# Kernel tuning notes

Measured on AMD Instinct MI355X. Metric: run time of the kernel, lower is better.

Reference implementation:

```python
import jax, jax.numpy as jnp
import numpy as np

B, N, R = 8, 1024, 8192
D_IN, REL_D = 32, 1
NF_P, NF_R, NF_E, D_OUT = 128, 128, 128, 3
PSTEP = 3


def setup_inputs() -> dict:
    key = jax.random.key(0)
    ks = jax.random.split(key, 26)
    state = jax.random.normal(ks[0], (B, N, D_IN), dtype=jnp.float32)
    # Rr/Rs are one-hot selection matrices [B, N, R]: column j selects the
    # receiver/sender particle of relation j.
    recv = jax.random.randint(ks[1], (B, R), 0, N)
    send = jax.random.randint(ks[2], (B, R), 0, N)
    Rr = jnp.transpose(jax.nn.one_hot(recv, N, dtype=jnp.float32), (0, 2, 1))
    Rs = jnp.transpose(jax.nn.one_hot(send, N, dtype=jnp.float32), (0, 2, 1))
    Ra = jax.random.normal(ks[3], (B, R, REL_D), dtype=jnp.float32)

    def lin(k, i, o):
        kw, kb = jax.random.split(k)
        return (0.02 * jax.random.normal(kw, (i, o), dtype=jnp.float32),
                0.02 * jax.random.normal(kb, (o,), dtype=jnp.float32))

    pe_w0, pe_b0 = lin(ks[4], D_IN, NF_P)
    pe_w1, pe_b1 = lin(ks[5], NF_P, NF_E)
    re_w0, re_b0 = lin(ks[6], 2 * D_IN + REL_D, NF_R)
    re_w1, re_b1 = lin(ks[7], NF_R, NF_R)
    re_w2, re_b2 = lin(ks[8], NF_R, NF_R)
    rp_w, rp_b = lin(ks[9], NF_R + 2 * NF_E, NF_E)   # relation_propagator
    pp_w, pp_b = lin(ks[10], 2 * NF_E, NF_E)          # particle_propagator
    pr_w0, pr_b0 = lin(ks[11], NF_E, NF_E)            # particle_predictor
    pr_w1, pr_b1 = lin(ks[12], NF_E, D_OUT)
    return dict(state=state, Rr=Rr, Rs=Rs, Ra=Ra, pstep=PSTEP,
                pe_w0=pe_w0, pe_b0=pe_b0, pe_w1=pe_w1, pe_b1=pe_b1,
                re_w0=re_w0, re_b0=re_b0, re_w1=re_w1, re_b1=re_b1,
                re_w2=re_w2, re_b2=re_b2, rp_w=rp_w, rp_b=rp_b,
                pp_w=pp_w, pp_b=pp_b, pr_w0=pr_w0, pr_b0=pr_b0,
                pr_w1=pr_w1, pr_b1=pr_b1)


def reference(state, Rr, Rs, Ra, pstep,
              pe_w0, pe_b0, pe_w1, pe_b1,
              re_w0, re_b0, re_w1, re_b1, re_w2, re_b2,
              rp_w, rp_b, pp_w, pp_b,
              pr_w0, pr_b0, pr_w1, pr_b1):
    relu = jax.nn.relu
    # gather particle states into relation slots: Rr^T @ state -> [B, R, D]
    state_r = jnp.einsum('bnr,bnd->brd', Rr, state)
    state_s = jnp.einsum('bnr,bnd->brd', Rs, state)
    # particle encoder: Linear-ReLU-Linear-ReLU
    particle_encode = relu(relu(state @ pe_w0 + pe_b0) @ pe_w1 + pe_b1)  # [B,N,NF_E]
    # relation encoder: 3-layer MLP with ReLU after each layer
    rel_in = jnp.concatenate([state_r, state_s, Ra], axis=2)
    h = relu(rel_in @ re_w0 + re_b0)
    h = relu(h @ re_w1 + re_b1)
    relation_encode = relu(h @ re_w2 + re_b2)  # [B,R,NF_R]

    particle_effect = jnp.zeros((B, N, NF_E), dtype=state.dtype)
    for _ in range(pstep):
        effect_r = jnp.einsum('bnr,bne->bre', Rr, particle_effect)  # gather
        effect_s = jnp.einsum('bnr,bne->bre', Rs, particle_effect)
        rel_x = jnp.concatenate([relation_encode, effect_r, effect_s], axis=2)
        relation_effect = relu(rel_x @ rp_w + rp_b)  # [B,R,NF_E]
        # scatter-add relation effects back to receiver particles
        effect_agg = jnp.einsum('bnr,bre->bne', Rr, relation_effect)
        part_x = jnp.concatenate([particle_encode, effect_agg], axis=2)
        # residual particle propagator: relu(linear(x) + prev_effect)
        particle_effect = relu(part_x @ pp_w + pp_b + particle_effect)
    pred = relu(particle_effect @ pr_w0 + pr_b0) @ pr_w1 + pr_b1  # [B,N,D_OUT]
    return pred
```

## Files before the change

kernel.cpp:

```cpp
#include <hip/hip_runtime.h>

#define NB 8
#define NP 1024
#define NR 8192

typedef unsigned short u16;
typedef __attribute__((ext_vector_type(8))) short bf16x8;
typedef __attribute__((ext_vector_type(4))) float f32x4;
typedef __attribute__((ext_vector_type(4))) unsigned int u32x4;

#define MFMA __builtin_amdgcn_mfma_f32_16x16x32_bf16

static __device__ __forceinline__ float bf2f(u16 u) {
    union { unsigned int i; float f; } v; v.i = ((unsigned int)u) << 16; return v.f;
}
static __device__ __forceinline__ unsigned int f2bf(float f) {
    union { float fv; unsigned int i; } v; v.fv = f;
    unsigned int r = v.i + 0x7FFFu + ((v.i >> 16) & 1u);
    return r >> 16;
}
static __device__ __forceinline__ unsigned int pack2(float a, float b) {
    return f2bf(a) | (f2bf(b) << 16);
}
static __device__ __forceinline__ void unpk8(uint4 v, float* o) {
    o[0] = bf2f((u16)(v.x & 0xFFFF)); o[1] = bf2f((u16)(v.x >> 16));
    o[2] = bf2f((u16)(v.y & 0xFFFF)); o[3] = bf2f((u16)(v.y >> 16));
    o[4] = bf2f((u16)(v.z & 0xFFFF)); o[5] = bf2f((u16)(v.z >> 16));
    o[6] = bf2f((u16)(v.w & 0xFFFF)); o[7] = bf2f((u16)(v.w >> 16));
}

__global__ __launch_bounds__(256) void k_idxprep(
    const u32x4* __restrict__ Rr4, const u32x4* __restrict__ Rs4,
    u16* __restrict__ recv, u16* __restrict__ send,
    const float* __restrict__ w0, const float* __restrict__ w1,
    const float* __restrict__ w2, const float* __restrict__ w3,
    const float* __restrict__ w4, const float* __restrict__ w5,
    const float* __restrict__ w6, const float* __restrict__ w7,
    bf16x8* __restrict__ wfrag)
{
    int tid = threadIdx.x;
    if (blockIdx.x < 8) {
        const float* W; int KC, kv, off;
        switch (blockIdx.x) {
            case 0:  W = w0; KC = 3;  kv = 65;  off = 0;  break;
            case 1:  W = w1; KC = 4;  kv = 128; off = 6;  break;
            case 2:  W = w2; KC = 4;  kv = 128; off = 14; break;
            case 3:  W = w3; KC = 1;  kv = 32;  off = 22; break;
            case 4:  W = w4; KC = 4;  kv = 128; off = 24; break;
            case 5:  W = w5; KC = 12; kv = 384; off = 32; break;
            case 6:  W = w6; KC = 8;  kv = 256; off = 56; break;
            default: W = w7; KC = 4;  kv = 128; off = 72; break;
        }
        int wave = tid >> 6, quad = (tid >> 4) & 3, l16 = tid & 15;
        for (int kc = 0; kc < KC; ++kc)
          for (int nt = 0; nt < 2; ++nt) {
            bf16x8 f;
            #pragma unroll
            for (int j = 0; j < 8; ++j) {
                int k = kc*32 + quad*8 + j;
                f[j] = (k < kv) ? (short)f2bf(W[k*128 + wave*32 + nt*16 + l16]) : (short)0;
            }
            wfrag[(off + kc*2 + nt)*256 + tid] = f;
          }
        return;
    }
    int sid = blockIdx.x - 8;
    int mat = sid & 1;
    const u32x4* src = mat ? Rs4 : Rr4;
    u16* dst = mat ? send : recv;
    long base = (long)(sid >> 1) * 512;
    long i0 = base + tid;
    long i1 = base + 256 + tid;
    u32x4 v0 = __builtin_nontemporal_load(src + i0);
    u32x4 v1 = __builtin_nontemporal_load(src + i1);
    {
        int c4 = (int)(i0 & 2047), n = (int)((i0 >> 11) & 1023), b = (int)(i0 >> 21);
        int o = b * NR + c4 * 4;
        if (v0[0]) dst[o + 0] = (u16)n;
        if (v0[1]) dst[o + 1] = (u16)n;
        if (v0[2]) dst[o + 2] = (u16)n;
        if (v0[3]) dst[o + 3] = (u16)n;
    }
    {
        int c4 = (int)(i1 & 2047), n = (int)((i1 >> 11) & 1023), b = (int)(i1 >> 21);
        int o = b * NR + c4 * 4;
        if (v1[0]) dst[o + 0] = (u16)n;
        if (v1[1]) dst[o + 1] = (u16)n;
        if (v1[2]) dst[o + 2] = (u16)n;
        if (v1[3]) dst[o + 3] = (u16)n;
    }
}

__global__ __launch_bounds__(1024) void k_csr(
    const u16* __restrict__ recv, const u16* __restrict__ send,
    int* __restrict__ row_ptr, u16* __restrict__ pos,
    u16* __restrict__ send_sorted)
{
    __shared__ int s[NP];
    __shared__ int cur[NP];
    int b = blockIdx.x, t = threadIdx.x;
    cur[t] = 0;
    __syncthreads();
    int pv[NR / 1024];
    #pragma unroll
    for (int k = 0; k < NR / 1024; ++k) {
        pv[k] = recv[b * NR + k * 1024 + t] & 1023;
        atomicAdd(&cur[pv[k]], 1);
    }
    __syncthreads();
    int v = cur[t];
    s[t] = v;
    __syncthreads();
    #pragma unroll
    for (int off = 1; off < NP; off <<= 1) {
        int add = (t >= off) ? s[t - off] : 0;
        __syncthreads();
        s[t] += add;
        __syncthreads();
    }
    int excl = s[t] - v;
    row_ptr[b * (NP + 1) + t] = excl;
    cur[t] = excl;
    if (t == NP - 1) row_ptr[b * (NP + 1) + NP] = s[t];
    __syncthreads();
    #pragma unroll
    for (int k = 0; k < NR / 1024; ++k) {
        int r = k * 1024 + t;
        int j = atomicAdd(&cur[pv[k]], 1) & 8191;
        pos[b * NR + r] = (u16)j;
        send_sorted[b * NR + j] = send[b * NR + r];
    }
}

template<int KC>
static __device__ __forceinline__ void load_wfrag(
    const bf16x8* __restrict__ fb, bf16x8 (&wf)[KC][2], int tid)
{
    #pragma unroll
    for (int kc = 0; kc < KC; ++kc)
      #pragma unroll
      for (int nt = 0; nt < 2; ++nt)
        wf[kc][nt] = fb[(kc*2 + nt)*256 + tid];
}

template<int MT, int KC, int LDA>
static __device__ __forceinline__ void mfma_compute(
    const u16* xlds, const bf16x8 (&wf)[KC][2], f32x4 (&acc)[MT][2],
    int l16, int quad)
{
    #pragma unroll
    for (int kc = 0; kc < KC; ++kc) {
        bf16x8 a[MT];
        #pragma unroll
        for (int mt = 0; mt < MT; ++mt)
            a[mt] = *(const bf16x8*)(xlds + (mt*16 + l16)*LDA + kc*32 + quad*8);
        #pragma unroll
        for (int mt = 0; mt < MT; ++mt) {
            acc[mt][0] = MFMA(a[mt], wf[kc][0], acc[mt][0], 0, 0, 0);
            acc[mt][1] = MFMA(a[mt], wf[kc][1], acc[mt][1], 0, 0, 0);
        }
    }
}

template<int MT>
static __device__ __forceinline__ void zero_acc(f32x4 (&acc)[MT][2]) {
    #pragma unroll
    for (int mt = 0; mt < MT; ++mt)
      #pragma unroll
      for (int nt = 0; nt < 2; ++nt)
        acc[mt][nt] = f32x4{0.f, 0.f, 0.f, 0.f};
}

template<int MT, int LDA>
static __device__ __forceinline__ void store_c_lds(
    u16* xlds, const f32x4 (&acc)[MT][2], const float* __restrict__ bias,
    int wave, int quad, int l16, int coloff = 0)
{
    #pragma unroll
    for (int mt = 0; mt < MT; ++mt)
      #pragma unroll
      for (int nt = 0; nt < 2; ++nt) {
        int col = wave*32 + nt*16 + l16;
        float bv = bias[col];
        #pragma unroll
        for (int rg = 0; rg < 4; ++rg)
            xlds[(mt*16 + quad*4 + rg)*LDA + coloff + col] =
                (u16)f2bf(fmaxf(acc[mt][nt][rg] + bv, 0.f));
      }
}

template<int MT, bool RELU>
static __device__ __forceinline__ void store_c_glob(
    u16* __restrict__ out, long row0, const f32x4 (&acc)[MT][2],
    const float* __restrict__ bias, int wave, int quad, int l16)
{
    #pragma unroll
    for (int mt = 0; mt < MT; ++mt)
      #pragma unroll
      for (int nt = 0; nt < 2; ++nt) {
        int col = wave*32 + nt*16 + l16;
        float bv = bias[col];
        #pragma unroll
        for (int rg = 0; rg < 4; ++rg) {
            long r = row0 + mt*16 + quad*4 + rg;
            float v = acc[mt][nt][rg] + bv;
            if (RELU) v = fmaxf(v, 0.f);
            out[r*128 + col] = (u16)f2bf(v);
        }
      }
}

__global__ __launch_bounds__(256) void k_encpe(
    const float* __restrict__ state, const float* __restrict__ Ra,
    const u16* __restrict__ recv, const u16* __restrict__ send,
    const u16* __restrict__ pos,
    const bf16x8* __restrict__ f_re0, const float* __restrict__ re_b0,
    const bf16x8* __restrict__ f_re1, const float* __restrict__ re_b1,
    const bf16x8* __restrict__ f_re2, const float* __restrict__ re_b2,
    const bf16x8* __restrict__ f_rpP, const float* __restrict__ rp_b,
    u16* __restrict__ bufP,
    const bf16x8* __restrict__ f_pe0, const float* __restrict__ pe_b0,
    const bf16x8* __restrict__ f_pe1, const float* __restrict__ pe_b1,
    u16* __restrict__ penc)
{
    constexpr int LDA = 136;
    __shared__ __align__(16) u16 xlds[64 * LDA];
    const int tid = threadIdx.x;
    const int wave = tid >> 6, quad = (tid >> 4) & 3, l16 = tid & 15;
    f32x4 acc[4][2];

    if (blockIdx.x < 1024) {
        const int row0 = blockIdx.x * 64;
        const int b = row0 >> 13;
        {
            int r = tid >> 2, tt = tid & 3;
            int rel = row0 + r;
            u16* dst = xlds + r * LDA;
            int ri = recv[rel] & 1023;
            int si = send[rel] & 1023;
            const float* rrow = state + ((long)(b*NP + ri)) * 32;
            const float* srow = state + ((long)(b*NP + si)) * 32;
            float4 a0 = *(const float4*)(rrow + tt*8);
            float4 a1 = *(const float4*)(rrow + tt*8 + 4);
            uint4 o;
            o.x = pack2(a0.x, a0.y); o.y = pack2(a0.z, a0.w);
            o.z = pack2(a1.x, a1.y); o.w = pack2(a1.z, a1.w);
            *(uint4*)(dst + tt*8) = o;
            float4 s0 = *(const float4*)(srow + tt*8);
            float4 s1 = *(const float4*)(srow + tt*8 + 4);
            o.x = pack2(s0.x, s0.y); o.y = pack2(s0.z, s0.w);
            o.z = pack2(s1.x, s1.y); o.w = pack2(s1.z, s1.w);
            *(uint4*)(dst + 32 + tt*8) = o;
            if (tt == 3) {
                uint4 z = make_uint4(0, 0, 0, 0);
                *(uint4*)(dst + 64) = z; *(uint4*)(dst + 72) = z;
                *(uint4*)(dst + 80) = z; *(uint4*)(dst + 88) = z;
                dst[64] = (u16)f2bf(Ra[rel]);
            }
        }
        __syncthreads();
        zero_acc<4>(acc);
        {
            bf16x8 wf[3][2];
            load_wfrag<3>(f_re0, wf, tid);
            mfma_compute<4, 3, LDA>(xlds, wf, acc, l16, quad);
        }
        __syncthreads();
        store_c_lds<4, LDA>(xlds, acc, re_b0, wave, quad, l16);
        __syncthreads();
        zero_acc<4>(acc);
        {
            bf16x8 wf[4][2];
            load_wfrag<4>(f_re1, wf, tid);
            mfma_compute<4, 4, LDA>(xlds, wf, acc, l16, quad);
        }
        __syncthreads();
        store_c_lds<4, LDA>(xlds, acc, re_b1, wave, quad, l16);
        __syncthreads();
        zero_acc<4>(acc);
        {
            bf16x8 wf[4][2];
            load_wfrag<4>(f_re2, wf, tid);
            mfma_compute<4, 4, LDA>(xlds, wf, acc, l16, quad);
        }
        __syncthreads();
        store_c_lds<4, LDA>(xlds, acc, re_b2, wave, quad, l16);
        __syncthreads();
        zero_acc<4>(acc);
        {
            bf16x8 wf[4][2];
            load_wfrag<4>(f_rpP, wf, tid);
            mfma_compute<4, 4, LDA>(xlds, wf, acc, l16, quad);
        }
        #pragma unroll
        for (int mt = 0; mt < 4; ++mt)
          #pragma unroll
          for (int nt = 0; nt < 2; ++nt) {
            int col = wave*32 + nt*16 + l16;
            float bv = rp_b[col];
            #pragma unroll
            for (int rg = 0; rg < 4; ++rg) {
                int rl = mt*16 + quad*4 + rg;
                int j = pos[row0 + rl] & 8191;
                bufP[((long)(b*NR + j))*128 + col] = (u16)f2bf(acc[mt][nt][rg] + bv);
            }
          }
    } else {
        const long row0 = (long)(blockIdx.x - 1024) * 64;
        for (int idx = tid; idx < 64 * 8; idx += 256) {
            int r = idx >> 3, c = idx & 7;
            float4 v = *(const float4*)(state + (row0 + r)*32 + c*4);
            uint2 o; o.x = pack2(v.x, v.y); o.y = pack2(v.z, v.w);
            *(uint2*)(xlds + r*LDA + c*4) = o;
        }
        __syncthreads();
        zero_acc<4>(acc);
        {
            bf16x8 wf[1][2];
            load_wfrag<1>(f_pe0, wf, tid);
            mfma_compute<4, 1, LDA>(xlds, wf, acc, l16, quad);
        }
        __syncthreads();
        store_c_lds<4, LDA>(xlds, acc, pe_b0, wave, quad, l16);
        __syncthreads();
        zero_acc<4>(acc);
        {
            bf16x8 wf[4][2];
            load_wfrag<4>(f_pe1, wf, tid);
            mfma_compute<4, 4, LDA>(xlds, wf, acc, l16, quad);
        }
        store_c_glob<4, true>(penc, row0, acc, pe_b1, wave, quad, l16);
    }
}

template<bool STEP1, bool MAKEUV, bool LAST>
__global__ __launch_bounds__(256) void k_pp(
    const u16* __restrict__ penc, const u16* __restrict__ bufP,
    const u16* __restrict__ UV_in, u16* __restrict__ UV_out,
    const int* __restrict__ row_ptr, const u16* __restrict__ send_sorted,
    const bf16x8* __restrict__ f_pp, const float* __restrict__ pp_b,
    const bf16x8* __restrict__ f_U, const bf16x8* __restrict__ f_V,
    const bf16x8* __restrict__ f_pr0, const float* __restrict__ pr_b0,
    const float* __restrict__ pr_w1, const float* __restrict__ pr_b1,
    float* __restrict__ peff32_io, float* __restrict__ out)
{
    constexpr int LDA = 264;
    __shared__ __align__(16) u16 xlds[32 * LDA];
    const int tid = threadIdx.x;
    const int wave = tid >> 6, quad = (tid >> 4) & 3, l16 = tid & 15;
    const long row0 = (long)blockIdx.x * 32;

    for (int idx = tid; idx < 512; idx += 256) {
        int r = idx >> 4, c = idx & 15;
        *(uint4*)(xlds + r*LDA + c*8) = *(const uint4*)(penc + (row0 + r)*128 + c*8);
    }
    {
        int pp = tid >> 3;
        int cq = tid & 7;
        int gp = (int)row0 + pp;
        int b = gp >> 10, pl = gp & 1023;
        const int* rp = row_ptr + b * (NP + 1);
        int s0 = rp[pl], e0 = rp[pl + 1];
        float a[16];
        #pragma unroll
        for (int t = 0; t < 16; ++t) a[t] = 0.f;
        float uv[16];
        if (!STEP1) {
            const u16* ur = UV_in + ((long)gp)*256 + cq*16;
            unpk8(*(const uint4*)ur, uv);
            unpk8(*(const uint4*)(ur + 8), uv + 8);
        }
        for (int j = s0; j < e0; ++j) {
            const u16* prow = bufP + ((long)(b*NR + j))*128 + cq*16;
            float pv[16];
            unpk8(*(const uint4*)prow, pv);
            unpk8(*(const uint4*)(prow + 8), pv + 8);
            if (STEP1) {
                #pragma unroll
                for (int e = 0; e < 16; ++e) a[e] += fmaxf(pv[e], 0.f);
            } else {
                int sj = send_sorted[b * NR + j] & 1023;
                const u16* vrow = UV_in + ((long)(b*NP + sj))*256 + 128 + cq*16;
                float vv[16];
                unpk8(*(const uint4*)vrow, vv);
                unpk8(*(const uint4*)(vrow + 8), vv + 8);
                #pragma unroll
                for (int e = 0; e < 16; ++e)
                    a[e] += fmaxf(pv[e] + uv[e] + vv[e], 0.f);
            }
        }
        u16* dst = xlds + pp*LDA + 128 + cq*16;
        uint4 o;
        o.x = pack2(a[0], a[1]);   o.y = pack2(a[2], a[3]);
        o.z = pack2(a[4], a[5]);   o.w = pack2(a[6], a[7]);
        *(uint4*)dst = o;
        o.x = pack2(a[8], a[9]);   o.y = pack2(a[10], a[11]);
        o.z = pack2(a[12], a[13]); o.w = pack2(a[14], a[15]);
        *(uint4*)(dst + 8) = o;
    }
    __syncthreads();

    f32x4 acc[2][2];
    {
        bf16x8 wf[8][2];
        load_wfrag<8>(f_pp, wf, tid);
        zero_acc<2>(acc);
        mfma_compute<2, 8, LDA>(xlds, wf, acc, l16, quad);
    }
    __syncthreads();

    #pragma unroll
    for (int mt = 0; mt < 2; ++mt)
      #pragma unroll
      for (int nt = 0; nt < 2; ++nt) {
        int col = wave*32 + nt*16 + l16;
        float bv = pp_b[col];
        #pragma unroll
        for (int rg = 0; rg < 4; ++rg) {
            int rloc = mt*16 + quad*4 + rg;
            long r = row0 + rloc;
            float prev = STEP1 ? 0.f : peff32_io[r*128 + col];
            float v = fmaxf(acc[mt][nt][rg] + bv + prev, 0.f);
            if (!LAST) peff32_io[r*128 + col] = v;
            xlds[rloc*LDA + col] = (u16)f2bf(v);
        }
      }
    __syncthreads();

    if (MAKEUV) {
        #pragma unroll
        for (int half = 0; half < 2; ++half) {
            bf16x8 wf[4][2];
            load_wfrag<4>(half ? f_V : f_U, wf, tid);
            zero_acc<2>(acc);
            mfma_compute<2, 4, LDA>(xlds, wf, acc, l16, quad);
            #pragma unroll
            for (int mt = 0; mt < 2; ++mt)
              #pragma unroll
              for (int nt = 0; nt < 2; ++nt) {
                int col = half*128 + wave*32 + nt*16 + l16;
                #pragma unroll
                for (int rg = 0; rg < 4; ++rg) {
                    long r = row0 + mt*16 + quad*4 + rg;
                    UV_out[r*256 + col] = (u16)f2bf(acc[mt][nt][rg]);
                }
              }
        }
    }
    if (LAST) {
        bf16x8 wf[4][2];
        load_wfrag<4>(f_pr0, wf, tid);
        zero_acc<2>(acc);
        mfma_compute<2, 4, LDA>(xlds, wf, acc, l16, quad);
        store_c_lds<2, LDA>(xlds, acc, pr_b0, wave, quad, l16, 128);
        __syncthreads();
        if (tid < 96) {
            int row = tid / 3, col = tid - row * 3;
            float s = pr_b1[col];
            const u16* hr = xlds + row * LDA + 128;
            #pragma unroll 8
            for (int k = 0; k < 128; ++k) s += bf2f(hr[k]) * pr_w1[k*3 + col];
            out[(row0 + row)*3 + col] = s;
        }
    }
}

extern "C" void kernel_launch(void* const* d_in, const int* in_sizes, int n_in,
                              void* d_out, int out_size, void* d_ws, size_t ws_size,
                              hipStream_t stream) {
    const float* state = (const float*)d_in[0];
    const float* Rr    = (const float*)d_in[1];
    const float* Rs    = (const float*)d_in[2];
    const float* Ra    = (const float*)d_in[3];
    const float* pe_w0 = (const float*)d_in[5];
    const float* pe_b0 = (const float*)d_in[6];
    const float* pe_w1 = (const float*)d_in[7];
    const float* pe_b1 = (const float*)d_in[8];
    const float* re_w0 = (const float*)d_in[9];
    const float* re_b0 = (const float*)d_in[10];
    const float* re_w1 = (const float*)d_in[11];
    const float* re_b1 = (const float*)d_in[12];
    const float* re_w2 = (const float*)d_in[13];
    const float* re_b2 = (const float*)d_in[14];
    const float* rp_w  = (const float*)d_in[15];
    const float* rp_b  = (const float*)d_in[16];
    const float* pp_w  = (const float*)d_in[17];
    const float* pp_b  = (const float*)d_in[18];
    const float* pr_w0 = (const float*)d_in[19];
    const float* pr_b0 = (const float*)d_in[20];
    const float* pr_w1 = (const float*)d_in[21];
    const float* pr_b1 = (const float*)d_in[22];

    char* p = (char*)d_ws;
    u16*    bufP    = (u16*)p;    p += (size_t)NB*NR*128*2;
    u16*    UVa     = (u16*)p;    p += (size_t)NB*NP*256*2;
    u16*    UVb     = (u16*)p;    p += (size_t)NB*NP*256*2;
    float*  peff32  = (float*)p;  p += (size_t)NB*NP*128*4;
    u16*    penc    = (u16*)p;    p += (size_t)NB*NP*128*2;
    bf16x8* wfrag   = (bf16x8*)p; p += (size_t)80*256*16;
    int*    row_ptr = (int*)p;    p += (size_t)NB*(NP+1)*4 + 12;
    u16*    recv    = (u16*)p;    p += (size_t)NB*NR*2;
    u16*    send    = (u16*)p;    p += (size_t)NB*NR*2;
    u16*    pos     = (u16*)p;    p += (size_t)NB*NR*2;
    u16*    send_s  = (u16*)p;    p += (size_t)NB*NR*2;

    const bf16x8* f_re0 = wfrag + 0*256;
    const bf16x8* f_re1 = wfrag + 6*256;
    const bf16x8* f_re2 = wfrag + 14*256;
    const bf16x8* f_pe0 = wfrag + 22*256;
    const bf16x8* f_pe1 = wfrag + 24*256;
    const bf16x8* f_rpP = wfrag + 32*256;
    const bf16x8* f_rpU = wfrag + 40*256;
    const bf16x8* f_rpV = wfrag + 48*256;
    const bf16x8* f_pp  = wfrag + 56*256;
    const bf16x8* f_pr0 = wfrag + 72*256;

    float* outp = (float*)d_out;

    k_idxprep<<<65544, 256, 0, stream>>>((const u32x4*)Rr, (const u32x4*)Rs, recv, send,
                                         re_w0, re_w1, re_w2, pe_w0, pe_w1, rp_w, pp_w, pr_w0,
                                         wfrag);
    k_csr<<<NB, 1024, 0, stream>>>(recv, send, row_ptr, pos, send_s);
    k_encpe<<<1152, 256, 0, stream>>>(state, Ra, recv, send, pos,
                                      f_re0, re_b0, f_re1, re_b1, f_re2, re_b2,
                                      f_rpP, rp_b, bufP,
                                      f_pe0, pe_b0, f_pe1, pe_b1, penc);
    k_pp<true,  true,  false><<<256, 256, 0, stream>>>(
        penc, bufP, UVa, UVa, row_ptr, send_s, f_pp, pp_b,
        f_rpU, f_rpV, f_pr0, pr_b0, pr_w1, pr_b1, peff32, outp);
    k_pp<false, true,  false><<<256, 256, 0, stream>>>(
        penc, bufP, UVa, UVb, row_ptr, send_s, f_pp, pp_b,
        f_rpU, f_rpV, f_pr0, pr_b0, pr_w1, pr_b1, peff32, outp);
    k_pp<false, false, true><<<256, 256, 0, stream>>>(
        penc, bufP, UVb, UVa, row_ptr, send_s, f_pp, pp_b,
        f_rpU, f_rpV, f_pr0, pr_b0, pr_w1, pr_b1, peff32, outp);
}
```

Baseline: 621.8 us.

## Move particle encoder into index-prep kernel and widen one-hot scan per block

Particle-encoder blocks move from the relation-encoder kernel into the index-prep kernel, converting fp32 weights to bf16 inline so they no longer depend on the packed weight fragments. The one-hot scan now has each block load 8 vectors per thread, which cuts the grid from about 65k to about 16k blocks. The CSR prefix scan switches from a shared-memory Hillis-Steele loop to wave shuffle scans. The propagation gather prefetches send indices eight at a time and broadcasts them with shuffles. The cost is more shared memory in the index-prep kernel, which may lower its occupancy.

```diff
diff --git a/kernel.cpp b/kernel.cpp
--- a/kernel.cpp
+++ b/kernel.cpp
@@ -27,6 +27,84 @@
     o[2] = bf2f((u16)(v.y & 0xFFFF)); o[3] = bf2f((u16)(v.y >> 16));
     o[4] = bf2f((u16)(v.z & 0xFFFF)); o[5] = bf2f((u16)(v.z >> 16));
     o[6] = bf2f((u16)(v.w & 0xFFFF)); o[7] = bf2f((u16)(v.w >> 16));
+}
+
+template<int KC>
+static __device__ __forceinline__ void load_wfrag(
+    const bf16x8* __restrict__ fb, bf16x8 (&wf)[KC][2], int tid)
+{
+    #pragma unroll
+    for (int kc = 0; kc < KC; ++kc)
+      #pragma unroll
+      for (int nt = 0; nt < 2; ++nt)
+        wf[kc][nt] = fb[(kc*2 + nt)*256 + tid];
+}
+
+template<int MT, int KC, int LDA>
+static __device__ __forceinline__ void mfma_compute(
+    const u16* xlds, const bf16x8 (&wf)[KC][2], f32x4 (&acc)[MT][2],
+    int l16, int quad)
+{
+    #pragma unroll
+    for (int kc = 0; kc < KC; ++kc) {
+        bf16x8 a[MT];
+        #pragma unroll
+        for (int mt = 0; mt < MT; ++mt)
+            a[mt] = *(const bf16x8*)(xlds + (mt*16 + l16)*LDA + kc*32 + quad*8);
+        #pragma unroll
+        for (int mt = 0; mt < MT; ++mt) {
+            acc[mt][0] = MFMA(a[mt], wf[kc][0], acc[mt][0], 0, 0, 0);
+            acc[mt][1] = MFMA(a[mt], wf[kc][1], acc[mt][1], 0, 0, 0);
+        }
+    }
+}
+
+template<int MT>
+static __device__ __forceinline__ void zero_acc(f32x4 (&acc)[MT][2]) {
+    #pragma unroll
+    for (int mt = 0; mt < MT; ++mt)
+      #pragma unroll
+      for (int nt = 0; nt < 2; ++nt)
+        acc[mt][nt] = f32x4{0.f, 0.f, 0.f, 0.f};
+}
+
+template<int MT, int LDA>
+static __device__ __forceinline__ void store_c_lds(
+    u16* xlds, const f32x4 (&acc)[MT][2], const float* __restrict__ bias,
+    int wave, int quad, int l16, int coloff = 0)
+{
+    #pragma unroll
+    for (int mt = 0; mt < MT; ++mt)
+      #pragma unroll
+      for (int nt = 0; nt < 2; ++nt) {
+        int col = wave*32 + nt*16 + l16;
+        float bv = bias[col];
+        #pragma unroll
+        for (int rg = 0; rg < 4; ++rg)
+            xlds[(mt*16 + quad*4 + rg)*LDA + coloff + col] =
+                (u16)f2bf(fmaxf(acc[mt][nt][rg] + bv, 0.f));
+      }
+}
+
+template<int MT, bool RELU>
+static __device__ __forceinline__ void store_c_glob(
+    u16* __restrict__ out, long row0, const f32x4 (&acc)[MT][2],
+    const float* __restrict__ bias, int wave, int quad, int l16)
+{
+    #pragma unroll
+    for (int mt = 0; mt < MT; ++mt)
+      #pragma unroll
+      for (int nt = 0; nt < 2; ++nt) {
+        int col = wave*32 + nt*16 + l16;
+        float bv = bias[col];
+        #pragma unroll
+        for (int rg = 0; rg < 4; ++rg) {
+            long r = row0 + mt*16 + quad*4 + rg;
+            float v = acc[mt][nt][rg] + bv;
+            if (RELU) v = fmaxf(v, 0.f);
+            out[r*128 + col] = (u16)f2bf(v);
+        }
+      }
 }
 
 __global__ __launch_bounds__(256) void k_idxprep(
@@ -36,9 +114,15 @@
     const float* __restrict__ w2, const float* __restrict__ w3,
     const float* __restrict__ w4, const float* __restrict__ w5,
     const float* __restrict__ w6, const float* __restrict__ w7,
-    bf16x8* __restrict__ wfrag)
-{
+    bf16x8* __restrict__ wfrag,
+    const float* __restrict__ state, const float* __restrict__ pe_b0,
+    const float* __restrict__ pe_b1, u16* __restrict__ penc)
+{
+    constexpr int LDA = 136;
+    __shared__ __align__(16) u16 xlds[64 * LDA];
     int tid = threadIdx.x;
+    const int wave = tid >> 6, quad = (tid >> 4) & 3, l16 = tid & 15;
+
     if (blockIdx.x < 8) {
         const float* W; int KC, kv, off;
         switch (blockIdx.x) {
@@ -51,7 +135,6 @@
             case 6:  W = w6; KC = 8;  kv = 256; off = 56; break;
             default: W = w7; KC = 4;  kv = 128; off = 72; break;
         }
-        int wave = tid >> 6, quad = (tid >> 4) & 3, l16 = tid & 15;
         for (int kc = 0; kc < KC; ++kc)
           for (int nt = 0; nt < 2; ++nt) {
             bf16x8 f;
@@ -64,30 +147,68 @@
           }
         return;
     }
-    int sid = blockIdx.x - 8;
+
+    if (blockIdx.x < 136) {
+        const long row0 = (long)(blockIdx.x - 8) * 64;
+        for (int idx = tid; idx < 64 * 8; idx += 256) {
+            int r = idx >> 3, c = idx & 7;
+            float4 v = *(const float4*)(state + (row0 + r)*32 + c*4);
+            uint2 o; o.x = pack2(v.x, v.y); o.y = pack2(v.z, v.w);
+            *(uint2*)(xlds + r*LDA + c*4) = o;
+        }
+        __syncthreads();
+        f32x4 acc[4][2];
+        zero_acc<4>(acc);
+        {
+            bf16x8 wf[1][2];
+            #pragma unroll
+            for (int nt = 0; nt < 2; ++nt)
+              #pragma unroll
+              for (int j = 0; j < 8; ++j) {
+                int k = quad*8 + j;
+                wf[0][nt][j] = (short)f2bf(w3[k*128 + wave*32 + nt*16 + l16]);
+              }
+            mfma_compute<4, 1, LDA>(xlds, wf, acc, l16, quad);
+        }
+        __syncthreads();
+        store_c_lds<4, LDA>(xlds, acc, pe_b0, wave, quad, l16);
+        __syncthreads();
+        zero_acc<4>(acc);
+        {
+            bf16x8 wf[4][2];
+            #pragma unroll
+            for (int kc = 0; kc < 4; ++kc)
+              #pragma unroll
+              for (int nt = 0; nt < 2; ++nt)
+                #pragma unroll
+                for (int j = 0; j < 8; ++j) {
+                    int k = kc*32 + quad*8 + j;
+                    wf[kc][nt][j] = (short)f2bf(w4[k*128 + wave*32 + nt*16 + l16]);
+                }
+            mfma_compute<4, 4, LDA>(xlds, wf, acc, l16, quad);
+        }
+        store_c_glob<4, true>(penc, row0, acc, pe_b1, wave, quad, l16);
+        return;
+    }
+
+    int sid = blockIdx.x - 136;
     int mat = sid & 1;
     const u32x4* src = mat ? Rs4 : Rr4;
     u16* dst = mat ? send : recv;
-    long base = (long)(sid >> 1) * 512;
-    long i0 = base + tid;
-    long i1 = base + 256 + tid;
-    u32x4 v0 = __builtin_nontemporal_load(src + i0);
-    u32x4 v1 = __builtin_nontemporal_load(src + i1);
-    {
-        int c4 = (int)(i0 & 2047), n = (int)((i0 >> 11) & 1023), b = (int)(i0 >> 21);
+    long base = (long)(sid >> 1) * 2048 + tid;
+    u32x4 v[8];
+    #pragma unroll
+    for (int k = 0; k < 8; ++k)
+        v[k] = __builtin_nontemporal_load(src + base + k*256);
+    #pragma unroll
+    for (int k = 0; k < 8; ++k) {
+        long i = base + k*256;
+        int c4 = (int)(i & 2047), n = (int)((i >> 11) & 1023), b = (int)(i >> 21);
         int o = b * NR + c4 * 4;
-        if (v0[0]) dst[o + 0] = (u16)n;
-        if (v0[1]) dst[o + 1] = (u16)n;
-        if (v0[2]) dst[o + 2] = (u16)n;
-        if (v0[3]) dst[o + 3] = (u16)n;
-    }
-    {
-        int c4 = (int)(i1 & 2047), n = (int)((i1 >> 11) & 1023), b = (int)(i1 >> 21);
-        int o = b * NR + c4 * 4;
-        if (v1[0]) dst[o + 0] = (u16)n;
-        if (v1[1]) dst[o + 1] = (u16)n;
-        if (v1[2]) dst[o + 2] = (u16)n;
-        if (v1[3]) dst[o + 3] = (u16)n;
+        if (v[k][0]) dst[o + 0] = (u16)n;
+        if (v[k][1]) dst[o + 1] = (u16)n;
+        if (v[k][2]) dst[o + 2] = (u16)n;
+        if (v[k][3]) dst[o + 3] = (u16)n;
     }
 }
 
@@ -96,8 +217,8 @@
     int* __restrict__ row_ptr, u16* __restrict__ pos,
     u16* __restrict__ send_sorted)
 {
-    __shared__ int s[NP];
     __shared__ int cur[NP];
+    __shared__ int wsum[16];
     int b = blockIdx.x, t = threadIdx.x;
     cur[t] = 0;
     __syncthreads();
@@ -109,19 +230,29 @@
     }
     __syncthreads();
     int v = cur[t];
-    s[t] = v;
-    __syncthreads();
-    #pragma unroll
-    for (int off = 1; off < NP; off <<= 1) {
-        int add = (t >= off) ? s[t - off] : 0;
-        __syncthreads();
-        s[t] += add;
-        __syncthreads();
-    }
-    int excl = s[t] - v;
+    int s = v;
+    #pragma unroll
+    for (int off = 1; off < 64; off <<= 1) {
+        int u = __shfl_up(s, off);
+        if ((t & 63) >= off) s += u;
+    }
+    if ((t & 63) == 63) wsum[t >> 6] = s;
+    __syncthreads();
+    if (t < 16) {
+        int ws = wsum[t];
+        int ss = ws;
+        #pragma unroll
+        for (int off = 1; off < 16; off <<= 1) {
+            int u = __shfl_up(ss, off);
+            if (t >= off) ss += u;
+        }
+        wsum[t] = ss - ws;
+    }
+    __syncthreads();
+    int excl = s - v + wsum[t >> 6];
     row_ptr[b * (NP + 1) + t] = excl;
     cur[t] = excl;
-    if (t == NP - 1) row_ptr[b * (NP + 1) + NP] = s[t];
+    if (t == NP - 1) row_ptr[b * (NP + 1) + NP] = excl + v;
     __syncthreads();
     #pragma unroll
     for (int k = 0; k < NR / 1024; ++k) {
@@ -132,85 +263,7 @@
     }
 }
 
-template<int KC>
-static __device__ __forceinline__ void load_wfrag(
-    const bf16x8* __restrict__ fb, bf16x8 (&wf)[KC][2], int tid)
-{
-    #pragma unroll
-    for (int kc = 0; kc < KC; ++kc)
-      #pragma unroll
-      for (int nt = 0; nt < 2; ++nt)
-        wf[kc][nt] = fb[(kc*2 + nt)*256 + tid];
-}
-
-template<int MT, int KC, int LDA>
-static __device__ __forceinline__ void mfma_compute(
-    const u16* xlds, const bf16x8 (&wf)[KC][2], f32x4 (&acc)[MT][2],
-    int l16, int quad)
-{
-    #pragma unroll
-    for (int kc = 0; kc < KC; ++kc) {
-        bf16x8 a[MT];
-        #pragma unroll
-        for (int mt = 0; mt < MT; ++mt)
-            a[mt] = *(const bf16x8*)(xlds + (mt*16 + l16)*LDA + kc*32 + quad*8);
-        #pragma unroll
-        for (int mt = 0; mt < MT; ++mt) {
-            acc[mt][0] = MFMA(a[mt], wf[kc][0], acc[mt][0], 0, 0, 0);
-            acc[mt][1] = MFMA(a[mt], wf[kc][1], acc[mt][1], 0, 0, 0);
-        }
-    }
-}
-
-template<int MT>
-static __device__ __forceinline__ void zero_acc(f32x4 (&acc)[MT][2]) {
-    #pragma unroll
-    for (int mt = 0; mt < MT; ++mt)
-      #pragma unroll
-      for (int nt = 0; nt < 2; ++nt)
-        acc[mt][nt] = f32x4{0.f, 0.f, 0.f, 0.f};
-}
-
-template<int MT, int LDA>
-static __device__ __forceinline__ void store_c_lds(
-    u16* xlds, const f32x4 (&acc)[MT][2], const float* __restrict__ bias,
-    int wave, int quad, int l16, int coloff = 0)
-{
-    #pragma unroll
-    for (int mt = 0; mt < MT; ++mt)
-      #pragma unroll
-      for (int nt = 0; nt < 2; ++nt) {
-        int col = wave*32 + nt*16 + l16;
-        float bv = bias[col];
-        #pragma unroll
-        for (int rg = 0; rg < 4; ++rg)
-            xlds[(mt*16 + quad*4 + rg)*LDA + coloff + col] =
-                (u16)f2bf(fmaxf(acc[mt][nt][rg] + bv, 0.f));
-      }
-}
-
-template<int MT, bool RELU>
-static __device__ __forceinline__ void store_c_glob(
-    u16* __restrict__ out, long row0, const f32x4 (&acc)[MT][2],
-    const float* __restrict__ bias, int wave, int quad, int l16)
-{
-    #pragma unroll
-    for (int mt = 0; mt < MT; ++mt)
-      #pragma unroll
-      for (int nt = 0; nt < 2; ++nt) {
-        int col = wave*32 + nt*16 + l16;
-        float bv = bias[col];
-        #pragma unroll
-        for (int rg = 0; rg < 4; ++rg) {
-            long r = row0 + mt*16 + quad*4 + rg;
-            float v = acc[mt][nt][rg] + bv;
-            if (RELU) v = fmaxf(v, 0.f);
-            out[r*128 + col] = (u16)f2bf(v);
-        }
-      }
-}
-
-__global__ __launch_bounds__(256) void k_encpe(
+__global__ __launch_bounds__(256) void k_encrel(
     const float* __restrict__ state, const float* __restrict__ Ra,
     const u16* __restrict__ recv, const u16* __restrict__ send,
     const u16* __restrict__ pos,
@@ -218,10 +271,7 @@
     const bf16x8* __restrict__ f_re1, const float* __restrict__ re_b1,
     const bf16x8* __restrict__ f_re2, const float* __restrict__ re_b2,
     const bf16x8* __restrict__ f_rpP, const float* __restrict__ rp_b,
-    u16* __restrict__ bufP,
-    const bf16x8* __restrict__ f_pe0, const float* __restrict__ pe_b0,
-    const bf16x8* __restrict__ f_pe1, const float* __restrict__ pe_b1,
-    u16* __restrict__ penc)
+    u16* __restrict__ bufP)
 {
     constexpr int LDA = 136;
     __shared__ __align__(16) u16 xlds[64 * LDA];
@@ -229,108 +279,81 @@
     const int wave = tid >> 6, quad = (tid >> 4) & 3, l16 = tid & 15;
     f32x4 acc[4][2];
 
-    if (blockIdx.x < 1024) {
-        const int row0 = blockIdx.x * 64;
-        const int b = row0 >> 13;
-        {
-            int r = tid >> 2, tt = tid & 3;
-            int rel = row0 + r;
-            u16* dst = xlds + r * LDA;
-            int ri = recv[rel] & 1023;
-            int si = send[rel] & 1023;
-            const float* rrow = state + ((long)(b*NP + ri)) * 32;
-            const float* srow = state + ((long)(b*NP + si)) * 32;
-            float4 a0 = *(const float4*)(rrow + tt*8);
-            float4 a1 = *(const float4*)(rrow + tt*8 + 4);
-            uint4 o;
-            o.x = pack2(a0.x, a0.y); o.y = pack2(a0.z, a0.w);
-            o.z = pack2(a1.x, a1.y); o.w = pack2(a1.z, a1.w);
-            *(uint4*)(dst + tt*8) = o;
-            float4 s0 = *(const float4*)(srow + tt*8);
-            float4 s1 = *(const float4*)(srow + tt*8 + 4);
-            o.x = pack2(s0.x, s0.y); o.y = pack2(s0.z, s0.w);
-            o.z = pack2(s1.x, s1.y); o.w = pack2(s1.z, s1.w);
-            *(uint4*)(dst + 32 + tt*8) = o;
-            if (tt == 3) {
-                uint4 z = make_uint4(0, 0, 0, 0);
-                *(uint4*)(dst + 64) = z; *(uint4*)(dst + 72) = z;
-                *(uint4*)(dst + 80) = z; *(uint4*)(dst + 88) = z;
-                dst[64] = (u16)f2bf(Ra[rel]);
-            }
-        }
-        __syncthreads();
-        zero_acc<4>(acc);
-        {
-            bf16x8 wf[3][2];
-            load_wfrag<3>(f_re0, wf, tid);
-            mfma_compute<4, 3, LDA>(xlds, wf, acc, l16, quad);
-        }
-        __syncthreads();
-        store_c_lds<4, LDA>(xlds, acc, re_b0, wave, quad, l16);
-        __syncthreads();
-        zero_acc<4>(acc);
-        {
-            bf16x8 wf[4][2];
-            load_wfrag<4>(f_re1, wf, tid);
-            mfma_compute<4, 4, LDA>(xlds, wf, acc, l16, quad);
-        }
-        __syncthreads();
-        store_c_lds<4, LDA>(xlds, acc, re_b1, wave, quad, l16);
-        __syncthreads();
-        zero_acc<4>(acc);
-        {
-            bf16x8 wf[4][2];
-            load_wfrag<4>(f_re2, wf, tid);
-            mfma_compute<4, 4, LDA>(xlds, wf, acc, l16, quad);
-        }
-        __syncthreads();
-        store_c_lds<4, LDA>(xlds, acc, re_b2, wave, quad, l16);
-        __syncthreads();
-        zero_acc<4>(acc);
-        {
-            bf16x8 wf[4][2];
-            load_wfrag<4>(f_rpP, wf, tid);
-            mfma_compute<4, 4, LDA>(xlds, wf, acc, l16, quad);
-        }
-        #pragma unroll
-        for (int mt = 0; mt < 4; ++mt)
-          #pragma unroll
-          for (int nt = 0; nt < 2; ++nt) {
-            int col = wave*32 + nt*16 + l16;
-            float bv = rp_b[col];
-            #pragma unroll
-            for (int rg = 0; rg < 4; ++rg) {
-                int rl = mt*16 + quad*4 + rg;
-                int j = pos[row0 + rl] & 8191;
-                bufP[((long)(b*NR + j))*128 + col] = (u16)f2bf(acc[mt][nt][rg] + bv);
-            }
-          }
-    } else {
-        const long row0 = (long)(blockIdx.x - 1024) * 64;
-        for (int idx = tid; idx < 64 * 8; idx += 256) {
-            int r = idx >> 3, c = idx & 7;
-            float4 v = *(const float4*)(state + (row0 + r)*32 + c*4);
-            uint2 o; o.x = pack2(v.x, v.y); o.y = pack2(v.z, v.w);
-            *(uint2*)(xlds + r*LDA + c*4) = o;
-        }
-        __syncthreads();
-        zero_acc<4>(acc);
-        {
-            bf16x8 wf[1][2];
-            load_wfrag<1>(f_pe0, wf, tid);
-            mfma_compute<4, 1, LDA>(xlds, wf, acc, l16, quad);
-        }
-        __syncthreads();
-        store_c_lds<4, LDA>(xlds, acc, pe_b0, wave, quad, l16);
-        __syncthreads();
-        zero_acc<4>(acc);
-        {
-            bf16x8 wf[4][2];
-            load_wfrag<4>(f_pe1, wf, tid);
-            mfma_compute<4, 4, LDA>(xlds, wf, acc, l16, quad);
-        }
-        store_c_glob<4, true>(penc, row0, acc, pe_b1, wave, quad, l16);
-    }
+    const int row0 = blockIdx.x * 64;
+    const int b = row0 >> 13;
+    {
+        int r = tid >> 2, tt = tid & 3;
+        int rel = row0 + r;
+        u16* dst = xlds + r * LDA;
+        int ri = recv[rel] & 1023;
+        int si = send[rel] & 1023;
+        const float* rrow = state + ((long)(b*NP + ri)) * 32;
+        const float* srow = state + ((long)(b*NP + si)) * 32;
+        float4 a0 = *(const float4*)(rrow + tt*8);
+        float4 a1 = *(const float4*)(rrow + tt*8 + 4);
+        uint4 o;
+        o.x = pack2(a0.x, a0.y); o.y = pack2(a0.z, a0.w);
+        o.z = pack2(a1.x, a1.y); o.w = pack2(a1.z, a1.w);
+        *(uint4*)(dst + tt*8) = o;
+        float4 s0 = *(const float4*)(srow + tt*8);
+        float4 s1 = *(const float4*)(srow + tt*8 + 4);
+        o.x = pack2(s0.x, s0.y); o.y = pack2(s0.z, s0.w);
+        o.z = pack2(s1.x, s1.y); o.w = pack2(s1.z, s1.w);
+        *(uint4*)(dst + 32 + tt*8) = o;
+        if (tt == 3) {
+            uint4 z = make_uint4(0, 0, 0, 0);
+            *(uint4*)(dst + 64) = z; *(uint4*)(dst + 72) = z;
+            *(uint4*)(dst + 80) = z; *(uint4*)(dst + 88) = z;
+            dst[64] = (u16)f2bf(Ra[rel]);
+        }
+    }
+    __syncthreads();
+    zero_acc<4>(acc);
+    {
+        bf16x8 wf[3][2];
+        load_wfrag<3>(f_re0, wf, tid);
+        mfma_compute<4, 3, LDA>(xlds, wf, acc, l16, quad);
+    }
+    __syncthreads();
+    store_c_lds<4, LDA>(xlds, acc, re_b0, wave, quad, l16);
+    __syncthreads();
+    zero_acc<4>(acc);
+    {
+        bf16x8 wf[4][2];
+        load_wfrag<4>(f_re1, wf, tid);
+        mfma_compute<4, 4, LDA>(xlds, wf, acc, l16, quad);
+    }
+    __syncthreads();
+    store_c_lds<4, LDA>(xlds, acc, re_b1, wave, quad, l16);
+    __syncthreads();
+    zero_acc<4>(acc);
+    {
+        bf16x8 wf[4][2];
+        load_wfrag<4>(f_re2, wf, tid);
+        mfma_compute<4, 4, LDA>(xlds, wf, acc, l16, quad);
+    }
+    __syncthreads();
+    store_c_lds<4, LDA>(xlds, acc, re_b2, wave, quad, l16);
+    __syncthreads();
+    zero_acc<4>(acc);
+    {
+        bf16x8 wf[4][2];
+        load_wfrag<4>(f_rpP, wf, tid);
+        mfma_compute<4, 4, LDA>(xlds, wf, acc, l16, quad);
+    }
+    #pragma unroll
+    for (int mt = 0; mt < 4; ++mt)
+      #pragma unroll
+      for (int nt = 0; nt < 2; ++nt) {
+        int col = wave*32 + nt*16 + l16;
+        float bv = rp_b[col];
+        #pragma unroll
+        for (int rg = 0; rg < 4; ++rg) {
+            int rl = mt*16 + quad*4 + rg;
+            int j = pos[row0 + rl] & 8191;
+            bufP[((long)(b*NR + j))*128 + col] = (u16)f2bf(acc[mt][nt][rg] + bv);
+        }
+      }
 }
 
 template<bool STEP1, bool MAKEUV, bool LAST>
@@ -370,23 +393,39 @@
             unpk8(*(const uint4*)ur, uv);
             unpk8(*(const uint4*)(ur + 8), uv + 8);
         }
-        for (int j = s0; j < e0; ++j) {
-            const u16* prow = bufP + ((long)(b*NR + j))*128 + cq*16;
-            float pv[16];
-            unpk8(*(const uint4*)prow, pv);
-            unpk8(*(const uint4*)(prow + 8), pv + 8);
-            if (STEP1) {
+        if (STEP1) {
+            for (int j = s0; j < e0; ++j) {
+                const u16* prow = bufP + ((long)(b*NR + j))*128 + cq*16;
+                float pv[16];
+                unpk8(*(const uint4*)prow, pv);
+                unpk8(*(const uint4*)(prow + 8), pv + 8);
                 #pragma unroll
                 for (int e = 0; e < 16; ++e) a[e] += fmaxf(pv[e], 0.f);
-            } else {
-                int sj = send_sorted[b * NR + j] & 1023;
-                const u16* vrow = UV_in + ((long)(b*NP + sj))*256 + 128 + cq*16;
-                float vv[16];
-                unpk8(*(const uint4*)vrow, vv);
-                unpk8(*(const uint4*)(vrow + 8), vv + 8);
-                #pragma unroll
-                for (int e = 0; e < 16; ++e)
-                    a[e] += fmaxf(pv[e] + uv[e] + vv[e], 0.f);
+            }
+        } else {
+            const int lane = tid & 63;
+            const int gb = lane & ~7;
+            const u16* ss_base = send_sorted + b * NR;
+            const u16* uvb = UV_in + ((long)(b*NP))*256 + 128 + cq*16;
+            for (int jb = s0; jb < e0; jb += 8) {
+                int jt = jb + (lane & 7);
+                int pre = (jt < e0) ? (int)ss_base[jt] : 0;
+                int m = e0 - jb; if (m > 8) m = 8;
+                for (int jj = 0; jj < m; ++jj) {
+                    int j = jb + jj;
+                    int sj = __shfl(pre, gb + jj) & 1023;
+                    const u16* prow = bufP + ((long)(b*NR + j))*128 + cq*16;
+                    float pv[16];
+                    unpk8(*(const uint4*)prow, pv);
+                    unpk8(*(const uint4*)(prow + 8), pv + 8);
+                    const u16* vrow = uvb + (long)sj*256;
+                    float vv[16];
+                    unpk8(*(const uint4*)vrow, vv);
+                    unpk8(*(const uint4*)(vrow + 8), vv + 8);
+                    #pragma unroll
+                    for (int e = 0; e < 16; ++e)
+                        a[e] += fmaxf(pv[e] + uv[e] + vv[e], 0.f);
+                }
             }
         }
         u16* dst = xlds + pp*LDA + 128 + cq*16;
@@ -507,8 +546,6 @@
     const bf16x8* f_re0 = wfrag + 0*256;
     const bf16x8* f_re1 = wfrag + 6*256;
     const bf16x8* f_re2 = wfrag + 14*256;
-    const bf16x8* f_pe0 = wfrag + 22*256;
-    const bf16x8* f_pe1 = wfrag + 24*256;
     const bf16x8* f_rpP = wfrag + 32*256;
     const bf16x8* f_rpU = wfrag + 40*256;
     const bf16x8* f_rpV = wfrag + 48*256;
@@ -517,14 +554,13 @@
 
     float* outp = (float*)d_out;
 
-    k_idxprep<<<65544, 256, 0, stream>>>((const u32x4*)Rr, (const u32x4*)Rs, recv, send,
+    k_idxprep<<<16520, 256, 0, stream>>>((const u32x4*)Rr, (const u32x4*)Rs, recv, send,
                                          re_w0, re_w1, re_w2, pe_w0, pe_w1, rp_w, pp_w, pr_w0,
-                                         wfrag);
+                                         wfrag, state, pe_b0, pe_b1, penc);
     k_csr<<<NB, 1024, 0, stream>>>(recv, send, row_ptr, pos, send_s);
-    k_encpe<<<1152, 256, 0, stream>>>(state, Ra, recv, send, pos,
-                                      f_re0, re_b0, f_re1, re_b1, f_re2, re_b2,
-                                      f_rpP, rp_b, bufP,
-                                      f_pe0, pe_b0, f_pe1, pe_b1, penc);
+    k_encrel<<<1024, 256, 0, stream>>>(state, Ra, recv, send, pos,
+                                       f_re0, re_b0, f_re1, re_b1, f_re2, re_b2,
+                                       f_rpP, rp_b, bufP);
     k_pp<true,  true,  false><<<256, 256, 0, stream>>>(
         penc, bufP, UVa, UVa, row_ptr, send_s, f_pp, pp_b,
         f_rpU, f_rpV, f_pr0, pr_b0, pr_w1, pr_b1, peff32, outp);
```

After: 614.4 us. No clear change (-1.2%).
